# Kernel tuning notes

Measured on AMD Instinct MI355X. Metric: run time of the kernel, lower is better.

The kernel has to match this reference:

```python
import jax, jax.numpy as jnp
import numpy as np
import math

B, H, S, D = 1, 8, 2048, 64
LAMBDA_INIT = 0.8 - 0.6 * math.exp(-0.3)  # depth=1
EPS = 1e-5


def _clin(xr, xi, wr, wi, br, bi):
    # complex linear: (wr + i*wi)(xr + i*xi)
    out_r = xr @ wr.T - xi @ wi.T + br
    out_i = xr @ wi.T + xi @ wr.T + bi
    return out_r, out_i


def setup_inputs() -> dict:
    ks = jax.random.split(jax.random.key(0), 24)
    n = lambda i, shp, s=1.0: jax.random.normal(ks[i], shp, jnp.float32) * s
    inv = 1.0 / math.sqrt(D)
    return {
        'q_r': n(0, (B, H, S, D)), 'q_i': n(1, (B, H, S, D)),
        'k_r': n(2, (B, H, S, D)), 'k_i': n(3, (B, H, S, D)),
        'v_r': n(4, (B, H, S, D)), 'v_i': n(5, (B, H, S, D)),
        'pe_q_r': n(6, (B, H, S, D)), 'pe_q_i': n(7, (B, H, S, D)),
        'pe_k_r': n(8, (B, H, S, D)), 'pe_k_i': n(9, (B, H, S, D)),
        'qwr': n(10, (2 * D, D), inv), 'qwi': n(11, (2 * D, D), inv),
        'qbr': jnp.zeros(2 * D), 'qbi': jnp.zeros(2 * D),
        'kwr': n(12, (D, D), inv), 'kwi': n(13, (D, D), inv),
        'kbr': jnp.zeros(D), 'kbi': jnp.zeros(D),
        'vwr': n(14, (D, D), inv), 'vwi': n(15, (D, D), inv),
        'vbr': jnp.zeros(D), 'vbi': jnp.zeros(D),
        'gwr': n(16, (D, D), inv), 'gwi': n(17, (D, D), inv),
        'gbr': jnp.zeros(D), 'gbi': jnp.zeros(D),
        'owr': n(18, (D, D), inv), 'owi': n(19, (D, D), inv),
        'obr': jnp.zeros(D), 'obi': jnp.zeros(D),
        'lq1': n(20, (H,), 0.1), 'lk1': n(21, (H,), 0.1),
        'lq2': n(22, (H,), 0.1), 'lk2': n(23, (H,), 0.1),
        'subw': jnp.ones(2 * D),
    }


def _forward(q_r, q_i, k_r, k_i, v_r, v_i, pe_q_r, pe_q_i, pe_k_r, pe_k_i,
             qwr, qwi, qbr, qbi, kwr, kwi, kbr, kbi, vwr, vwi, vbr, vbi,
             gwr, gwi, gbr, gbi, owr, owi, obr, obi,
             lq1, lk1, lq2, lk2, subw):
    b, h, s, d = q_r.shape
    scale = d ** (-0.5)
    qpr, qpi = _clin(q_r, q_i, qwr, qwi, qbr, qbi)      # [b,h,s,2d]
    kpr, kpi = _clin(k_r, k_i, kwr, kwi, kbr, kbi)      # [b,h,s,d]
    vpr, vpi = _clin(v_r, v_i, vwr, vwi, vbr, vbi)      # [b,h,s,d]
    qpr = qpr + jnp.concatenate([pe_q_r, pe_q_r], -1)
    qpi = qpi + jnp.concatenate([pe_q_i, pe_q_i], -1)
    kpr = kpr + pe_k_r
    kpi = kpi + pe_k_i
    # split two physical heads: view(..., d, 2) interleaves last dim
    qpr = qpr.reshape(b, h, s, d, 2)
    qpi = qpi.reshape(b, h, s, d, 2)
    q1r, q2r = qpr[..., 0], qpr[..., 1]
    q1i, q2i = qpi[..., 0], qpi[..., 1]

    def attn(qr, qi):
        sr = jnp.einsum('bhqd,bhkd->bhqk', qr, kpr) + jnp.einsum('bhqd,bhkd->bhqk', qi, kpi)
        si = jnp.einsum('bhqd,bhkd->bhqk', qi, kpr) - jnp.einsum('bhqd,bhkd->bhqk', qr, kpi)
        scores = jnp.sqrt(sr * sr + si * si + 1e-8) * scale
        return jax.nn.softmax(scores, axis=-1)

    a1 = attn(q1r, q1i)
    a2 = attn(q2r, q2i)
    o1r = a1 @ vpr; o1i = a1 @ vpi
    o2r = a2 @ vpr; o2i = a2 @ vpi
    # NOTE: torch computes a lambda-weighted difference here but immediately
    # overwrites it with the normed slice below, so it never reaches the output.
    cr = jnp.stack([o1r, o2r], -1).reshape(b, h, s, 2 * d)
    ci = jnp.stack([o1i, o2i], -1).reshape(b, h, s, 2 * d)
    rms = jnp.sqrt(jnp.mean(cr * cr + ci * ci, axis=-1, keepdims=True) + EPS)
    nr = cr / rms * subw
    ni = ci / rms * subw
    ar = nr[..., :d]
    ai = ni[..., :d]
    gr, gi = _clin(q_r, q_i, gwr, gwi, gbr, gbi)
    xr = gr * ar - gi * ai
    xi = gr * ai + gi * ar
    out_r, out_i = _clin(xr, xi, owr, owi, obr, obi)
    return out_r, out_i, gr, gi


def reference(q_r, q_i, k_r, k_i, v_r, v_i, pe_q_r, pe_q_i, pe_k_r, pe_k_i,
              qwr, qwi, qbr, qbi, kwr, kwi, kbr, kbi, vwr, vwi, vbr, vbi,
              gwr, gwi, gbr, gbi, owr, owi, obr, obi,
              lq1, lk1, lq2, lk2, subw):
    return _forward(q_r, q_i, k_r, k_i, v_r, v_i, pe_q_r, pe_q_i, pe_k_r, pe_k_i,
                    qwr, qwi, qbr, qbi, kwr, kwi, kbr, kbi, vwr, vwi, vbr, vbi,
                    gwr, gwi, gbr, gbi, owr, owi, obr, obi,
                    lq1, lk1, lq2, lk2, subw)
```

## Files before the change

### kernel.cpp

```cpp
#include <hip/hip_runtime.h>
#include <hip/hip_bf16.h>

#define NH 8
#define SQ 2048
#define HD 64
#define NTOT (NH * SQ * HD)

typedef unsigned short u16;
typedef unsigned int u32;
typedef __attribute__((ext_vector_type(8))) unsigned short us8;
typedef __attribute__((ext_vector_type(4))) unsigned short us4v;
typedef __attribute__((ext_vector_type(8))) _Float16 h8;
typedef __attribute__((ext_vector_type(4))) float f4;
typedef __attribute__((ext_vector_type(4))) u32 u4;

#define MFMA_F16 __builtin_amdgcn_mfma_f32_16x16x32_f16

__device__ __forceinline__ u16 f2h(float f) {
    union { _Float16 h; u16 u; } c; c.h = (_Float16)f; return c.u;
}
__device__ __forceinline__ float h2f(u16 u) {
    union { _Float16 h; u16 u; } c; c.u = u; return (float)c.h;
}
__device__ __forceinline__ h8 neg_h8(h8 a) {
    union { h8 h; u4 u; } c; c.h = a;
    c.u ^= 0x80008000u;
    return c.h;
}
__device__ __forceinline__ h8 pack8h(const float* p) {
    float4 a = ((const float4*)p)[0];
    float4 b = ((const float4*)p)[1];
    h8 r;
    r[0] = (_Float16)a.x; r[1] = (_Float16)a.y; r[2] = (_Float16)a.z; r[3] = (_Float16)a.w;
    r[4] = (_Float16)b.x; r[5] = (_Float16)b.y; r[6] = (_Float16)b.z; r[7] = (_Float16)b.w;
    return r;
}

__device__ __forceinline__ int swz8(int row, int chunk) {
    return row * 64 + ((chunk ^ (row & 7)) << 3);
}

struct Afrag { h8 r0, r1, i0, i1, ni0, ni1; };

__global__ __launch_bounds__(128) void prep1_kernel(
    const float* __restrict__ qwr, const float* __restrict__ qwi,
    const float* __restrict__ kwr, const float* __restrict__ kwi,
    const float* __restrict__ vwr, const float* __restrict__ vwi,
    const float* __restrict__ gwr, const float* __restrict__ gwi,
    u16* __restrict__ pk)
{
    const int b = blockIdx.x;
    const float* W; int nt;
    if (b < 8)       { W = qwr; nt = b; }
    else if (b < 16) { W = qwi; nt = b - 8; }
    else if (b < 20) { W = kwr; nt = b - 16; }
    else if (b < 24) { W = kwi; nt = b - 20; }
    else if (b < 28) { W = vwr; nt = b - 24; }
    else if (b < 32) { W = vwi; nt = b - 28; }
    else if (b < 36) { W = gwr; nt = b - 32; }
    else             { W = gwi; nt = b - 36; }
    const int t = threadIdx.x, hf = t >> 6, l = t & 63;
    const int quad = l >> 4, m16 = l & 15;
    h8 v = pack8h(W + (nt * 16 + m16) * 64 + hf * 32 + quad * 8);
    *(h8*)(pk + b * 1024 + hf * 512 + l * 8) = v;
}

__global__ __launch_bounds__(128) void prep2_kernel(
    const float* __restrict__ owr, const float* __restrict__ owi,
    u16* __restrict__ pk)
{
    const int b = blockIdx.x;
    const float* W = (b < 4) ? owr : owi;
    const int nt = b & 3;
    const int t = threadIdx.x, hf = t >> 6, l = t & 63;
    const int quad = l >> 4, m16 = l & 15;
    h8 v = pack8h(W + (nt * 16 + m16) * 64 + hf * 32 + quad * 8);
    *(h8*)(pk + b * 1024 + hf * 512 + l * 8) = v;
}

__global__ __launch_bounds__(256) void proj_kernel(
    const float* __restrict__ q_r, const float* __restrict__ q_i,
    const float* __restrict__ k_r, const float* __restrict__ k_i,
    const float* __restrict__ v_r, const float* __restrict__ v_i,
    const float* __restrict__ pe_q_r, const float* __restrict__ pe_q_i,
    const float* __restrict__ pe_k_r, const float* __restrict__ pe_k_i,
    const u16* __restrict__ pk,
    const float* __restrict__ qbr, const float* __restrict__ qbi,
    const float* __restrict__ kbr, const float* __restrict__ kbi,
    const float* __restrict__ vbr, const float* __restrict__ vbi,
    const float* __restrict__ gbr, const float* __restrict__ gbi,
    u16* __restrict__ q1r, u16* __restrict__ q1i,
    u16* __restrict__ q2r, u16* __restrict__ q2i,
    u16* __restrict__ kpr, u16* __restrict__ kpi,
    u16* __restrict__ vtr, u16* __restrict__ vti,
    float* __restrict__ out_gr, float* __restrict__ out_gi)
{
    __shared__ __align__(16) u16 Sqr[16 * 64], Sqi[16 * 64];
    __shared__ __align__(16) u16 Skr[16 * 64], Ski[16 * 64];
    __shared__ __align__(16) u16 Svr[16 * 64], Svi[16 * 64];

    const int t = threadIdx.x;
    const int wv = t >> 6, l = t & 63;
    const int quad = l >> 4, m16 = l & 15;
    const int rowbase = blockIdx.x * 16;
    const int h = rowbase >> 11;
    const int l8 = l * 8;

    {
        const int r = t >> 4, c4 = (t & 15) * 4;
        const int off = swz8(r, c4 >> 3) + (c4 & 7);
        const size_t gi = (size_t)(rowbase + r) * 64 + c4;
        auto stage = [&](const float* src, u16* dst) {
            float4 v = *(const float4*)(src + gi);
            us4v p;
            p[0] = f2h(v.x); p[1] = f2h(v.y); p[2] = f2h(v.z); p[3] = f2h(v.w);
            *(us4v*)&dst[off] = p;
        };
        stage(q_r, Sqr); stage(q_i, Sqi);
        stage(k_r, Skr); stage(k_i, Ski);
        stage(v_r, Svr); stage(v_i, Svi);
    }
    __syncthreads();

    auto loadA = [&](const u16* Sr, const u16* Si) {
        Afrag a;
        a.r0 = *(const h8*)&Sr[swz8(m16, quad)];
        a.r1 = *(const h8*)&Sr[swz8(m16, quad + 4)];
        a.i0 = *(const h8*)&Si[swz8(m16, quad)];
        a.i1 = *(const h8*)&Si[swz8(m16, quad + 4)];
        a.ni0 = neg_h8(a.i0);
        a.ni1 = neg_h8(a.i1);
        return a;
    };

    auto ctile = [&](const Afrag& A, int planeR, int planeI, f4& Cr, f4& Ci) {
        const u16* pR = pk + planeR * 1024;
        const u16* pI = pk + planeI * 1024;
        h8 Br0 = *(const h8*)(pR + l8);
        h8 Br1 = *(const h8*)(pR + 512 + l8);
        h8 Bi0 = *(const h8*)(pI + l8);
        h8 Bi1 = *(const h8*)(pI + 512 + l8);
        Cr = (f4)0.f; Ci = (f4)0.f;
        Cr = MFMA_F16(A.r0,  Br0, Cr, 0, 0, 0);
        Cr = MFMA_F16(A.r1,  Br1, Cr, 0, 0, 0);
        Cr = MFMA_F16(A.ni0, Bi0, Cr, 0, 0, 0);
        Cr = MFMA_F16(A.ni1, Bi1, Cr, 0, 0, 0);
        Ci = MFMA_F16(A.r0,  Bi0, Ci, 0, 0, 0);
        Ci = MFMA_F16(A.r1,  Bi1, Ci, 0, 0, 0);
        Ci = MFMA_F16(A.i0,  Br0, Ci, 0, 0, 0);
        Ci = MFMA_F16(A.i1,  Br1, Ci, 0, 0, 0);
    };

    auto qtile = [&](const Afrag& A, int nt) {
        f4 Cr, Ci;
        ctile(A, nt, 8 + nt, Cr, Ci);
        int c = nt * 16 + m16;
        float br = qbr[c], bi = qbi[c];
        int dd = c >> 1, pc = c & 63;
        u16* dR = (c & 1) ? q2r : q1r;
        u16* dI = (c & 1) ? q2i : q1i;
        #pragma unroll
        for (int r = 0; r < 4; ++r) {
            int g = rowbase + quad * 4 + r;
            dR[g * 64 + dd] = f2h(Cr[r] + br + pe_q_r[g * 64 + pc]);
            dI[g * 64 + dd] = f2h(Ci[r] + bi + pe_q_i[g * 64 + pc]);
        }
    };
    auto ktile = [&](const Afrag& A, int nt) {
        f4 Cr, Ci;
        ctile(A, 16 + nt, 20 + nt, Cr, Ci);
        int c = nt * 16 + m16;
        float br = kbr[c], bi = kbi[c];
        #pragma unroll
        for (int r = 0; r < 4; ++r) {
            int g = rowbase + quad * 4 + r;
            kpr[g * 64 + c] = f2h(Cr[r] + br + pe_k_r[g * 64 + c]);
            kpi[g * 64 + c] = f2h(Ci[r] + bi + pe_k_i[g * 64 + c]);
        }
    };
    auto vtile = [&](const Afrag& A, int nt) {
        f4 Cr, Ci;
        ctile(A, 24 + nt, 28 + nt, Cr, Ci);
        int c = nt * 16 + m16;
        float br = vbr[c], bi = vbi[c];
        int s0 = (rowbase & 2047) + quad * 4;
        size_t tix = (size_t)(h * 64 + c) * 2048 + s0;
        us4v pr, pi;
        #pragma unroll
        for (int r = 0; r < 4; ++r) {
            pr[r] = f2h(Cr[r] + br);
            pi[r] = f2h(Ci[r] + bi);
        }
        *(us4v*)&vtr[tix] = pr;
        *(us4v*)&vti[tix] = pi;
    };
    auto gtile = [&](const Afrag& A, int nt) {
        f4 Cr, Ci;
        ctile(A, 32 + nt, 36 + nt, Cr, Ci);
        int c = nt * 16 + m16;
        float br = gbr[c], bi = gbi[c];
        #pragma unroll
        for (int r = 0; r < 4; ++r) {
            int g = rowbase + quad * 4 + r;
            out_gr[g * 64 + c] = Cr[r] + br;
            out_gi[g * 64 + c] = Ci[r] + bi;
        }
    };

    if (wv == 0) {
        Afrag Aq = loadA(Sqr, Sqi);
        qtile(Aq, 0); qtile(Aq, 1); qtile(Aq, 2); qtile(Aq, 3); qtile(Aq, 4);
    } else if (wv == 1) {
        Afrag Aq = loadA(Sqr, Sqi);
        qtile(Aq, 5); qtile(Aq, 6); qtile(Aq, 7);
        gtile(Aq, 0); gtile(Aq, 1);
    } else if (wv == 2) {
        Afrag Ak = loadA(Skr, Ski);
        ktile(Ak, 0); ktile(Ak, 1); ktile(Ak, 2); ktile(Ak, 3);
        Afrag Aq = loadA(Sqr, Sqi);
        gtile(Aq, 2);
    } else {
        Afrag Av = loadA(Svr, Svi);
        vtile(Av, 0); vtile(Av, 1); vtile(Av, 2); vtile(Av, 3);
        Afrag Aq = loadA(Sqr, Sqi);
        gtile(Aq, 3);
    }
}

__global__ __launch_bounds__(512, 2) void attn_kernel(
    const u16* __restrict__ q1r, const u16* __restrict__ q1i,
    const u16* __restrict__ q2r, const u16* __restrict__ q2i,
    const u16* __restrict__ kpr, const u16* __restrict__ kpi,
    const u16* __restrict__ vtr, const u16* __restrict__ vti,
    u16* __restrict__ o1r, u16* __restrict__ o1i,
    u16* __restrict__ o2r, u16* __restrict__ o2i)
{
    __shared__ __align__(16) u16 Kr[2][64 * 64], Ki[2][64 * 64];
    __shared__ __align__(16) u16 Vr[2][64 * 64], Vi[2][64 * 64];
    __shared__ __align__(16) u16 Pb[128 * 64];

    const int t  = threadIdx.x;
    const int qt = blockIdx.x;
    const int h  = blockIdx.z;

    const int wq   = t >> 6;
    const int br   = wq >> 2;
    const int wr   = wq & 3;
    const int l    = t & 63;
    const int quad = l >> 4;
    const int m    = l & 15;

    const u16* Qsr = br ? q2r : q1r;
    const u16* Qsi = br ? q2i : q1i;
    const int hbase = h * SQ * 64;
    const int qbase = hbase + qt * 64 * 64;
    const int vbase = h * 64 * SQ;

    const u16* qrr = Qsr + qbase + (wr * 16 + m) * 64;
    const u16* qri = Qsi + qbase + (wr * 16 + m) * 64;
    h8 Qr0 = *(const h8*)(qrr + quad * 8);
    h8 Qr1 = *(const h8*)(qrr + 32 + quad * 8);
    h8 Qi0 = *(const h8*)(qri + quad * 8);
    h8 Qi1 = *(const h8*)(qri + 32 + quad * 8);
    h8 nQr0 = neg_h8(Qr0);
    h8 nQr1 = neg_h8(Qr1);

    const int sr0 = t >> 3;
    const int sc  = t & 7;
    us8 rK, rC, rV, rW;

    auto issue = [&](int kt) {
        const int kb = hbase + kt * 4096;
        const int vb = vbase + kt * 64;
        const int sc8 = sc * 8;
        rK = *(const us8*)(kpr + kb + sr0 * 64 + sc8);
        rC = *(const us8*)(kpi + kb + sr0 * 64 + sc8);
        rV = *(const us8*)(vtr + vb + sr0 * SQ + sc8);
        rW = *(const us8*)(vti + vb + sr0 * SQ + sc8);
    };
    auto commit = [&](int b) {
        const int o = swz8(sr0, sc);
        *(us8*)&Kr[b][o] = rK;
        *(us8*)&Ki[b][o] = rC;
        *(us8*)&Vr[b][o] = rV;
        *(us8*)&Vi[b][o] = rW;
    };

    float mreg[4], Lp[4];
    #pragma unroll
    for (int r = 0; r < 4; ++r) { mreg[r] = -1e30f; Lp[r] = 0.f; }
    f4 Ovr[4], Ovi[4];
    #pragma unroll
    for (int d = 0; d < 4; ++d) { Ovr[d] = (f4)0.f; Ovi[d] = (f4)0.f; }

    issue(0);
    commit(0);
    issue(1);
    __syncthreads();

    for (int kt = 0; kt < 32; ++kt) {
        const int cur = kt & 1;
        if (kt < 31) commit(cur ^ 1);
        if (kt < 30) issue(kt + 2);

        float sv[4][4];
        #pragma unroll
        for (int nt = 0; nt < 4; ++nt) {
            const int kr = nt * 16 + m;
            h8 k0 = *(const h8*)&Kr[cur][swz8(kr, quad)];
            h8 k1 = *(const h8*)&Kr[cur][swz8(kr, quad + 4)];
            h8 c0 = *(const h8*)&Ki[cur][swz8(kr, quad)];
            h8 c1 = *(const h8*)&Ki[cur][swz8(kr, quad + 4)];
            f4 ar = (f4)0.f, ai = (f4)0.f;
            __builtin_amdgcn_s_setprio(1);
            ar = MFMA_F16(Qr0, k0, ar, 0, 0, 0);
            ar = MFMA_F16(Qr1, k1, ar, 0, 0, 0);
            ar = MFMA_F16(Qi0, c0, ar, 0, 0, 0);
            ar = MFMA_F16(Qi1, c1, ar, 0, 0, 0);
            ai = MFMA_F16(Qi0, k0, ai, 0, 0, 0);
            ai = MFMA_F16(Qi1, k1, ai, 0, 0, 0);
            ai = MFMA_F16(nQr0, c0, ai, 0, 0, 0);
            ai = MFMA_F16(nQr1, c1, ai, 0, 0, 0);
            __builtin_amdgcn_s_setprio(0);
            #pragma unroll
            for (int r = 0; r < 4; ++r)
                sv[nt][r] = __builtin_amdgcn_sqrtf(ar[r] * ar[r] + ai[r] * ai[r] + 1e-8f) * 0.125f;
        }

        float rv[4];
        #pragma unroll
        for (int r = 0; r < 4; ++r) {
            float x = fmaxf(fmaxf(sv[0][r], sv[1][r]), fmaxf(sv[2][r], sv[3][r]));
            x = fmaxf(x, __shfl_xor(x, 1));
            x = fmaxf(x, __shfl_xor(x, 2));
            x = fmaxf(x, __shfl_xor(x, 4));
            x = fmaxf(x, __shfl_xor(x, 8));
            rv[r] = x;
        }

        bool need = (rv[0] > mreg[0] + 8.f) | (rv[1] > mreg[1] + 8.f) |
                    (rv[2] > mreg[2] + 8.f) | (rv[3] > mreg[3] + 8.f);
        if (__any(need)) {
            #pragma unroll
            for (int r = 0; r < 4; ++r) {
                float mn = fmaxf(mreg[r], rv[r]);
                float al = __expf(mreg[r] - mn);
                mreg[r] = mn;
                Lp[r] *= al;
                #pragma unroll
                for (int dtr = 0; dtr < 4; ++dtr) { Ovr[dtr][r] *= al; Ovi[dtr][r] *= al; }
            }
        }

        #pragma unroll
        for (int r = 0; r < 4; ++r) {
            const int prow = wq * 16 + quad * 4 + r;
            #pragma unroll
            for (int nt = 0; nt < 4; ++nt) {
                float p = __expf(sv[nt][r] - mreg[r]);
                Lp[r] += p;
                const int col = nt * 16 + m;
                Pb[swz8(prow, col >> 3) + (col & 7)] = f2h(p);
            }
        }

        const int qrow = wq * 16 + m;
        h8 pa0 = *(const h8*)&Pb[swz8(qrow, quad)];
        h8 pa1 = *(const h8*)&Pb[swz8(qrow, quad + 4)];

        #pragma unroll
        for (int dt = 0; dt < 4; ++dt) {
            const int vr_ = dt * 16 + m;
            h8 b0 = *(const h8*)&Vr[cur][swz8(vr_, quad)];
            h8 b1 = *(const h8*)&Vr[cur][swz8(vr_, quad + 4)];
            h8 d0 = *(const h8*)&Vi[cur][swz8(vr_, quad)];
            h8 d1 = *(const h8*)&Vi[cur][swz8(vr_, quad + 4)];
            __builtin_amdgcn_s_setprio(1);
            Ovr[dt] = MFMA_F16(pa0, b0, Ovr[dt], 0, 0, 0);
            Ovr[dt] = MFMA_F16(pa1, b1, Ovr[dt], 0, 0, 0);
            Ovi[dt] = MFMA_F16(pa0, d0, Ovi[dt], 0, 0, 0);
            Ovi[dt] = MFMA_F16(pa1, d1, Ovi[dt], 0, 0, 0);
            __builtin_amdgcn_s_setprio(0);
        }

        __syncthreads();
    }

    {
        #pragma unroll
        for (int r = 0; r < 4; ++r) {
            float x = Lp[r];
            x += __shfl_xor(x, 1);
            x += __shfl_xor(x, 2);
            x += __shfl_xor(x, 4);
            x += __shfl_xor(x, 8);
            Lp[r] = x;
        }
        u16* Dr = br ? o2r : o1r;
        u16* Di = br ? o2i : o1i;
        float inv[4];
        #pragma unroll
        for (int r = 0; r < 4; ++r) inv[r] = 1.f / Lp[r];
        #pragma unroll
        for (int dt = 0; dt < 4; ++dt) {
            #pragma unroll
            for (int r = 0; r < 4; ++r) {
                int q = wr * 16 + quad * 4 + r;
                Dr[qbase + q * 64 + dt * 16 + m] = f2h(Ovr[dt][r] * inv[r]);
                Di[qbase + q * 64 + dt * 16 + m] = f2h(Ovi[dt][r] * inv[r]);
            }
        }
    }
}

__global__ __launch_bounds__(256) void epi_kernel(
    const u16* __restrict__ o1r, const u16* __restrict__ o1i,
    const u16* __restrict__ o2r, const u16* __restrict__ o2i,
    const float* __restrict__ out_gr, const float* __restrict__ out_gi,
    const float* __restrict__ subw,
    const u16* __restrict__ pko,
    const float* __restrict__ obr, const float* __restrict__ obi,
    float* __restrict__ out_r, float* __restrict__ out_i)
{
    __shared__ __align__(16) u16 L1r[16][64], L1i[16][64];
    __shared__ __align__(16) u16 L2r[16][64], L2i[16][64];
    __shared__ __align__(16) u16 Xr[16 * 64], Xi[16 * 64];

    const int t = threadIdx.x;
    const int rowbase = blockIdx.x * 16;

    {
        int r = t >> 4, c4 = (t & 15) * 4;
        size_t gi = (size_t)(rowbase + r) * 64 + c4;
        *(us4v*)&L1r[r][c4] = *(const us4v*)(o1r + gi);
        *(us4v*)&L1i[r][c4] = *(const us4v*)(o1i + gi);
        *(us4v*)&L2r[r][c4] = *(const us4v*)(o2r + gi);
        *(us4v*)&L2i[r][c4] = *(const us4v*)(o2i + gi);
    }
    __syncthreads();

    {
        int r = t >> 4, c4 = (t & 15) * 4;
        float ss = 0.f;
        #pragma unroll
        for (int j = 0; j < 4; ++j) {
            float a = h2f(L1r[r][c4 + j]), b = h2f(L1i[r][c4 + j]);
            float c = h2f(L2r[r][c4 + j]), d = h2f(L2i[r][c4 + j]);
            ss += a * a + b * b + c * c + d * d;
        }
        ss += __shfl_xor(ss, 1);
        ss += __shfl_xor(ss, 2);
        ss += __shfl_xor(ss, 4);
        ss += __shfl_xor(ss, 8);
        float inv = 1.f / sqrtf(ss * (1.f / 128.f) + 1e-5f);

        float4 g_r = *(const float4*)(out_gr + (size_t)(rowbase + r) * 64 + c4);
        float4 g_i = *(const float4*)(out_gi + (size_t)(rowbase + r) * 64 + c4);
        const float* grv = (const float*)&g_r;
        const float* giv = (const float*)&g_i;

        us4v xrp, xip;
        #pragma unroll
        for (int j = 0; j < 4; ++j) {
            int c = c4 + j;
            int s = c >> 1;
            float cr_ = (c & 1) ? h2f(L2r[r][s]) : h2f(L1r[r][s]);
            float ci_ = (c & 1) ? h2f(L2i[r][s]) : h2f(L1i[r][s]);
            float sw = subw[c];
            float ar_ = cr_ * inv * sw;
            float ai_ = ci_ * inv * sw;
            xrp[j] = f2h(grv[j] * ar_ - giv[j] * ai_);
            xip[j] = f2h(grv[j] * ai_ + giv[j] * ar_);
        }
        const int off = swz8(r, c4 >> 3) + (c4 & 7);
        *(us4v*)&Xr[off] = xrp;
        *(us4v*)&Xi[off] = xip;
    }
    __syncthreads();

    const int wv = t >> 6, l = t & 63;
    const int quad = l >> 4, m16 = l & 15;
    const int l8 = l * 8;

    h8 Ar0 = *(const h8*)&Xr[swz8(m16, quad)];
    h8 Ar1 = *(const h8*)&Xr[swz8(m16, quad + 4)];
    h8 Ai0 = *(const h8*)&Xi[swz8(m16, quad)];
    h8 Ai1 = *(const h8*)&Xi[swz8(m16, quad + 4)];
    h8 nAi0 = neg_h8(Ai0), nAi1 = neg_h8(Ai1);

    const int c = wv * 16 + m16;
    h8 Br0 = *(const h8*)(pko + wv * 1024 + l8);
    h8 Br1 = *(const h8*)(pko + wv * 1024 + 512 + l8);
    h8 Bi0 = *(const h8*)(pko + 4096 + wv * 1024 + l8);
    h8 Bi1 = *(const h8*)(pko + 4096 + wv * 1024 + 512 + l8);

    f4 Cr = (f4)0.f, Ci = (f4)0.f;
    Cr = MFMA_F16(Ar0,  Br0, Cr, 0, 0, 0);
    Cr = MFMA_F16(Ar1,  Br1, Cr, 0, 0, 0);
    Cr = MFMA_F16(nAi0, Bi0, Cr, 0, 0, 0);
    Cr = MFMA_F16(nAi1, Bi1, Cr, 0, 0, 0);
    Ci = MFMA_F16(Ar0,  Bi0, Ci, 0, 0, 0);
    Ci = MFMA_F16(Ar1,  Bi1, Ci, 0, 0, 0);
    Ci = MFMA_F16(Ai0,  Br0, Ci, 0, 0, 0);
    Ci = MFMA_F16(Ai1,  Br1, Ci, 0, 0, 0);

    float br_ = obr[c], bi_ = obi[c];
    #pragma unroll
    for (int r = 0; r < 4; ++r) {
        size_t g = (size_t)(rowbase + quad * 4 + r) * 64 + c;
        out_r[g] = Cr[r] + br_;
        out_i[g] = Ci[r] + bi_;
    }
}

extern "C" void kernel_launch(void* const* d_in, const int* in_sizes, int n_in,
                              void* d_out, int out_size, void* d_ws, size_t ws_size,
                              hipStream_t stream)
{
    (void)in_sizes; (void)n_in; (void)out_size; (void)ws_size;

    float* out    = (float*)d_out;
    float* out_r  = out;
    float* out_i  = out + (size_t)NTOT;
    float* out_gr = out + 2 * (size_t)NTOT;
    float* out_gi = out + 3 * (size_t)NTOT;

    char* w = (char*)d_ws;
    const size_t N = (size_t)NTOT;
    u16* q1r = (u16*)w; w += N * 2;
    u16* q1i = (u16*)w; w += N * 2;
    u16* q2r = (u16*)w; w += N * 2;
    u16* q2i = (u16*)w; w += N * 2;
    u16* kpr = (u16*)w; w += N * 2;
    u16* kpi = (u16*)w; w += N * 2;
    u16* vtr = (u16*)w; w += N * 2;
    u16* vti = (u16*)w; w += N * 2;
    u16* o1r = (u16*)w; w += N * 2;
    u16* o1i = (u16*)w; w += N * 2;
    u16* o2r = (u16*)w; w += N * 2;
    u16* o2i = (u16*)w; w += N * 2;

    u16* pk1 = o1r;
    u16* pk2 = q1r;

    prep1_kernel<<<dim3(40), dim3(128), 0, stream>>>(
        (const float*)d_in[10], (const float*)d_in[11],
        (const float*)d_in[14], (const float*)d_in[15],
        (const float*)d_in[18], (const float*)d_in[19],
        (const float*)d_in[22], (const float*)d_in[23],
        pk1);

    proj_kernel<<<dim3(1024), dim3(256), 0, stream>>>(
        (const float*)d_in[0], (const float*)d_in[1],
        (const float*)d_in[2], (const float*)d_in[3],
        (const float*)d_in[4], (const float*)d_in[5],
        (const float*)d_in[6], (const float*)d_in[7],
        (const float*)d_in[8], (const float*)d_in[9],
        pk1,
        (const float*)d_in[12], (const float*)d_in[13],
        (const float*)d_in[16], (const float*)d_in[17],
        (const float*)d_in[20], (const float*)d_in[21],
        (const float*)d_in[24], (const float*)d_in[25],
        q1r, q1i, q2r, q2i, kpr, kpi, vtr, vti, out_gr, out_gi);

    attn_kernel<<<dim3(SQ / 64, 1, NH), dim3(512), 0, stream>>>(
        q1r, q1i, q2r, q2i, kpr, kpi, vtr, vti, o1r, o1i, o2r, o2i);

    prep2_kernel<<<dim3(8), dim3(128), 0, stream>>>(
        (const float*)d_in[26], (const float*)d_in[27], pk2);

    epi_kernel<<<dim3(1024), dim3(256), 0, stream>>>(
        o1r, o1i, o2r, o2i, out_gr, out_gi,
        (const float*)d_in[34], pk2,
        (const float*)d_in[28], (const float*)d_in[29],
        out_r, out_i);
}
```

Measured before the change: 236.1 us.

## Split KV tiles across two wave groups with 32-row waves and merged softmax

Each wave now handles 32 query rows instead of 16, so every K/V fragment read from LDS feeds twice as many MFMAs. The two halves of the block process alternating KV tiles from a triple-buffered LDS ring and merge their partial max, sum and output through LDS scratch at the end. This aims to cut LDS read traffic per MFMA and expose more independent work. In exchange, LDS use grows to about 128KB, which likely allows only one block per CU despite the launch bound of 2, and each iteration now has an extra barrier.

```diff
diff --git a/kernel.cpp b/kernel.cpp
--- a/kernel.cpp
+++ b/kernel.cpp
@@ -235,17 +235,17 @@
     u16* __restrict__ o1r, u16* __restrict__ o1i,
     u16* __restrict__ o2r, u16* __restrict__ o2i)
 {
-    __shared__ __align__(16) u16 Kr[2][64 * 64], Ki[2][64 * 64];
-    __shared__ __align__(16) u16 Vr[2][64 * 64], Vi[2][64 * 64];
-    __shared__ __align__(16) u16 Pb[128 * 64];
+    __shared__ __align__(16) u16 TILE[3][4][4096];
+    __shared__ __align__(16) u16 Pb[256 * 64];
 
     const int t  = threadIdx.x;
     const int qt = blockIdx.x;
     const int h  = blockIdx.z;
 
     const int wq   = t >> 6;
-    const int br   = wq >> 2;
-    const int wr   = wq & 3;
+    const int grp  = wq >> 2;
+    const int br   = (wq >> 1) & 1;
+    const int rh   = wq & 1;
     const int l    = t & 63;
     const int quad = l >> 4;
     const int m    = l & 15;
@@ -256,158 +256,232 @@
     const int qbase = hbase + qt * 64 * 64;
     const int vbase = h * 64 * SQ;
 
-    const u16* qrr = Qsr + qbase + (wr * 16 + m) * 64;
-    const u16* qri = Qsi + qbase + (wr * 16 + m) * 64;
-    h8 Qr0 = *(const h8*)(qrr + quad * 8);
-    h8 Qr1 = *(const h8*)(qrr + 32 + quad * 8);
-    h8 Qi0 = *(const h8*)(qri + quad * 8);
-    h8 Qi1 = *(const h8*)(qri + 32 + quad * 8);
-    h8 nQr0 = neg_h8(Qr0);
-    h8 nQr1 = neg_h8(Qr1);
+    h8 Qr0[2], Qr1[2], Qi0[2], Qi1[2];
+    #pragma unroll
+    for (int rs = 0; rs < 2; ++rs) {
+        const u16* qrr = Qsr + qbase + (rh * 32 + rs * 16 + m) * 64;
+        const u16* qri = Qsi + qbase + (rh * 32 + rs * 16 + m) * 64;
+        Qr0[rs] = *(const h8*)(qrr + quad * 8);
+        Qr1[rs] = *(const h8*)(qrr + 32 + quad * 8);
+        Qi0[rs] = *(const h8*)(qri + quad * 8);
+        Qi1[rs] = *(const h8*)(qri + 32 + quad * 8);
+    }
 
     const int sr0 = t >> 3;
     const int sc  = t & 7;
-    us8 rK, rC, rV, rW;
-
-    auto issue = [&](int kt) {
+    us8 rKa, rCa, rVa, rWa;
+    us8 rKb, rCb, rVb, rWb;
+
+    auto issueT = [&](int kt, us8& K, us8& C, us8& V, us8& W) {
         const int kb = hbase + kt * 4096;
         const int vb = vbase + kt * 64;
         const int sc8 = sc * 8;
-        rK = *(const us8*)(kpr + kb + sr0 * 64 + sc8);
-        rC = *(const us8*)(kpi + kb + sr0 * 64 + sc8);
-        rV = *(const us8*)(vtr + vb + sr0 * SQ + sc8);
-        rW = *(const us8*)(vti + vb + sr0 * SQ + sc8);
-    };
-    auto commit = [&](int b) {
+        K = *(const us8*)(kpr + kb + sr0 * 64 + sc8);
+        C = *(const us8*)(kpi + kb + sr0 * 64 + sc8);
+        V = *(const us8*)(vtr + vb + sr0 * SQ + sc8);
+        W = *(const us8*)(vti + vb + sr0 * SQ + sc8);
+    };
+    auto commitT = [&](int slot, const us8& K, const us8& C, const us8& V, const us8& W) {
         const int o = swz8(sr0, sc);
-        *(us8*)&Kr[b][o] = rK;
-        *(us8*)&Ki[b][o] = rC;
-        *(us8*)&Vr[b][o] = rV;
-        *(us8*)&Vi[b][o] = rW;
-    };
-
-    float mreg[4], Lp[4];
+        *(us8*)&TILE[slot][0][o] = K;
+        *(us8*)&TILE[slot][1][o] = C;
+        *(us8*)&TILE[slot][2][o] = V;
+        *(us8*)&TILE[slot][3][o] = W;
+    };
+
+    float mreg[2][4], Lp[2][4];
     #pragma unroll
-    for (int r = 0; r < 4; ++r) { mreg[r] = -1e30f; Lp[r] = 0.f; }
-    f4 Ovr[4], Ovi[4];
+    for (int rs = 0; rs < 2; ++rs)
+        #pragma unroll
+        for (int r = 0; r < 4; ++r) { mreg[rs][r] = -1e30f; Lp[rs][r] = 0.f; }
+    f4 Ovr[2][4], Ovi[2][4];
     #pragma unroll
-    for (int d = 0; d < 4; ++d) { Ovr[d] = (f4)0.f; Ovi[d] = (f4)0.f; }
-
-    issue(0);
-    commit(0);
-    issue(1);
+    for (int rs = 0; rs < 2; ++rs)
+        #pragma unroll
+        for (int d = 0; d < 4; ++d) { Ovr[rs][d] = (f4)0.f; Ovi[rs][d] = (f4)0.f; }
+
+    issueT(0, rKa, rCa, rVa, rWa);
+    issueT(1, rKb, rCb, rVb, rWb);
+    commitT(0, rKa, rCa, rVa, rWa);
+    issueT(2, rKa, rCa, rVa, rWa);
+    commitT(1, rKb, rCb, rVb, rWb);
+    issueT(3, rKb, rCb, rVb, rWb);
     __syncthreads();
 
-    for (int kt = 0; kt < 32; ++kt) {
-        const int cur = kt & 1;
-        if (kt < 31) commit(cur ^ 1);
-        if (kt < 30) issue(kt + 2);
-
-        float sv[4][4];
+    for (int s = 0; s < 16; ++s) {
+        const int myt  = 2 * s + grp;
+        const int slot = myt % 3;
+        if (s < 15) commitT((2 * s + 2) % 3, rKa, rCa, rVa, rWa);
+        if (s < 14) issueT(2 * s + 4, rKa, rCa, rVa, rWa);
+
+        const u16* Kr_ = TILE[slot][0];
+        const u16* Ki_ = TILE[slot][1];
+        const u16* Vr_ = TILE[slot][2];
+        const u16* Vi_ = TILE[slot][3];
+
+        float sv[2][4][4];
         #pragma unroll
         for (int nt = 0; nt < 4; ++nt) {
             const int kr = nt * 16 + m;
-            h8 k0 = *(const h8*)&Kr[cur][swz8(kr, quad)];
-            h8 k1 = *(const h8*)&Kr[cur][swz8(kr, quad + 4)];
-            h8 c0 = *(const h8*)&Ki[cur][swz8(kr, quad)];
-            h8 c1 = *(const h8*)&Ki[cur][swz8(kr, quad + 4)];
-            f4 ar = (f4)0.f, ai = (f4)0.f;
+            h8 k0 = *(const h8*)&Kr_[swz8(kr, quad)];
+            h8 k1 = *(const h8*)&Kr_[swz8(kr, quad + 4)];
+            h8 c0 = *(const h8*)&Ki_[swz8(kr, quad)];
+            h8 c1 = *(const h8*)&Ki_[swz8(kr, quad + 4)];
+            h8 nc0 = neg_h8(c0);
+            h8 nc1 = neg_h8(c1);
             __builtin_amdgcn_s_setprio(1);
-            ar = MFMA_F16(Qr0, k0, ar, 0, 0, 0);
-            ar = MFMA_F16(Qr1, k1, ar, 0, 0, 0);
-            ar = MFMA_F16(Qi0, c0, ar, 0, 0, 0);
-            ar = MFMA_F16(Qi1, c1, ar, 0, 0, 0);
-            ai = MFMA_F16(Qi0, k0, ai, 0, 0, 0);
-            ai = MFMA_F16(Qi1, k1, ai, 0, 0, 0);
-            ai = MFMA_F16(nQr0, c0, ai, 0, 0, 0);
-            ai = MFMA_F16(nQr1, c1, ai, 0, 0, 0);
+            #pragma unroll
+            for (int rs = 0; rs < 2; ++rs) {
+                f4 ar = (f4)0.f, ai = (f4)0.f;
+                ar = MFMA_F16(Qr0[rs], k0, ar, 0, 0, 0);
+                ar = MFMA_F16(Qr1[rs], k1, ar, 0, 0, 0);
+                ar = MFMA_F16(Qi0[rs], c0, ar, 0, 0, 0);
+                ar = MFMA_F16(Qi1[rs], c1, ar, 0, 0, 0);
+                ai = MFMA_F16(Qi0[rs], k0, ai, 0, 0, 0);
+                ai = MFMA_F16(Qi1[rs], k1, ai, 0, 0, 0);
+                ai = MFMA_F16(Qr0[rs], nc0, ai, 0, 0, 0);
+                ai = MFMA_F16(Qr1[rs], nc1, ai, 0, 0, 0);
+                #pragma unroll
+                for (int r = 0; r < 4; ++r)
+                    sv[rs][nt][r] =
+                        __builtin_amdgcn_sqrtf(ar[r] * ar[r] + ai[r] * ai[r] + 1e-8f) * 0.125f;
+            }
             __builtin_amdgcn_s_setprio(0);
-            #pragma unroll
-            for (int r = 0; r < 4; ++r)
-                sv[nt][r] = __builtin_amdgcn_sqrtf(ar[r] * ar[r] + ai[r] * ai[r] + 1e-8f) * 0.125f;
-        }
-
-        float rv[4];
-        #pragma unroll
-        for (int r = 0; r < 4; ++r) {
-            float x = fmaxf(fmaxf(sv[0][r], sv[1][r]), fmaxf(sv[2][r], sv[3][r]));
-            x = fmaxf(x, __shfl_xor(x, 1));
-            x = fmaxf(x, __shfl_xor(x, 2));
-            x = fmaxf(x, __shfl_xor(x, 4));
-            x = fmaxf(x, __shfl_xor(x, 8));
-            rv[r] = x;
-        }
-
-        bool need = (rv[0] > mreg[0] + 8.f) | (rv[1] > mreg[1] + 8.f) |
-                    (rv[2] > mreg[2] + 8.f) | (rv[3] > mreg[3] + 8.f);
+        }
+
+        float rv[2][4];
+        bool need = false;
+        #pragma unroll
+        for (int rs = 0; rs < 2; ++rs)
+            #pragma unroll
+            for (int r = 0; r < 4; ++r) {
+                float x = fmaxf(fmaxf(sv[rs][0][r], sv[rs][1][r]),
+                                fmaxf(sv[rs][2][r], sv[rs][3][r]));
+                x = fmaxf(x, __shfl_xor(x, 1));
+                x = fmaxf(x, __shfl_xor(x, 2));
+                x = fmaxf(x, __shfl_xor(x, 4));
+                x = fmaxf(x, __shfl_xor(x, 8));
+                rv[rs][r] = x;
+                need |= (x > mreg[rs][r] + 8.f);
+            }
         if (__any(need)) {
             #pragma unroll
+            for (int rs = 0; rs < 2; ++rs)
+                #pragma unroll
+                for (int r = 0; r < 4; ++r) {
+                    float mn = fmaxf(mreg[rs][r], rv[rs][r]);
+                    float al = __expf(mreg[rs][r] - mn);
+                    mreg[rs][r] = mn;
+                    Lp[rs][r] *= al;
+                    #pragma unroll
+                    for (int dt = 0; dt < 4; ++dt) {
+                        Ovr[rs][dt][r] *= al; Ovi[rs][dt][r] *= al;
+                    }
+                }
+        }
+
+        #pragma unroll
+        for (int rs = 0; rs < 2; ++rs)
+            #pragma unroll
             for (int r = 0; r < 4; ++r) {
-                float mn = fmaxf(mreg[r], rv[r]);
-                float al = __expf(mreg[r] - mn);
-                mreg[r] = mn;
-                Lp[r] *= al;
+                const int prow = wq * 32 + rs * 16 + quad * 4 + r;
                 #pragma unroll
-                for (int dtr = 0; dtr < 4; ++dtr) { Ovr[dtr][r] *= al; Ovi[dtr][r] *= al; }
+                for (int nt = 0; nt < 4; ++nt) {
+                    float p = __expf(sv[rs][nt][r] - mreg[rs][r]);
+                    Lp[rs][r] += p;
+                    const int col = nt * 16 + m;
+                    Pb[swz8(prow, col >> 3) + (col & 7)] = f2h(p);
+                }
             }
-        }
-
-        #pragma unroll
-        for (int r = 0; r < 4; ++r) {
-            const int prow = wq * 16 + quad * 4 + r;
-            #pragma unroll
-            for (int nt = 0; nt < 4; ++nt) {
-                float p = __expf(sv[nt][r] - mreg[r]);
-                Lp[r] += p;
-                const int col = nt * 16 + m;
-                Pb[swz8(prow, col >> 3) + (col & 7)] = f2h(p);
+
+        h8 pa0[2], pa1[2];
+        #pragma unroll
+        for (int rs = 0; rs < 2; ++rs) {
+            const int qrow = wq * 32 + rs * 16 + m;
+            pa0[rs] = *(const h8*)&Pb[swz8(qrow, quad)];
+            pa1[rs] = *(const h8*)&Pb[swz8(qrow, quad + 4)];
+        }
+
+        #pragma unroll
+        for (int dt = 0; dt < 4; ++dt) {
+            const int vrr = dt * 16 + m;
+            h8 b0 = *(const h8*)&Vr_[swz8(vrr, quad)];
+            h8 b1 = *(const h8*)&Vr_[swz8(vrr, quad + 4)];
+            h8 d0 = *(const h8*)&Vi_[swz8(vrr, quad)];
+            h8 d1 = *(const h8*)&Vi_[swz8(vrr, quad + 4)];
+            __builtin_amdgcn_s_setprio(1);
+            #pragma unroll
+            for (int rs = 0; rs < 2; ++rs) {
+                Ovr[rs][dt] = MFMA_F16(pa0[rs], b0, Ovr[rs][dt], 0, 0, 0);
+                Ovr[rs][dt] = MFMA_F16(pa1[rs], b1, Ovr[rs][dt], 0, 0, 0);
+                Ovi[rs][dt] = MFMA_F16(pa0[rs], d0, Ovi[rs][dt], 0, 0, 0);
+                Ovi[rs][dt] = MFMA_F16(pa1[rs], d1, Ovi[rs][dt], 0, 0, 0);
             }
-        }
-
-        const int qrow = wq * 16 + m;
-        h8 pa0 = *(const h8*)&Pb[swz8(qrow, quad)];
-        h8 pa1 = *(const h8*)&Pb[swz8(qrow, quad + 4)];
-
-        #pragma unroll
-        for (int dt = 0; dt < 4; ++dt) {
-            const int vr_ = dt * 16 + m;
-            h8 b0 = *(const h8*)&Vr[cur][swz8(vr_, quad)];
-            h8 b1 = *(const h8*)&Vr[cur][swz8(vr_, quad + 4)];
-            h8 d0 = *(const h8*)&Vi[cur][swz8(vr_, quad)];
-            h8 d1 = *(const h8*)&Vi[cur][swz8(vr_, quad + 4)];
-            __builtin_amdgcn_s_setprio(1);
-            Ovr[dt] = MFMA_F16(pa0, b0, Ovr[dt], 0, 0, 0);
-            Ovr[dt] = MFMA_F16(pa1, b1, Ovr[dt], 0, 0, 0);
-            Ovi[dt] = MFMA_F16(pa0, d0, Ovi[dt], 0, 0, 0);
-            Ovi[dt] = MFMA_F16(pa1, d1, Ovi[dt], 0, 0, 0);
             __builtin_amdgcn_s_setprio(0);
         }
 
         __syncthreads();
-    }
-
-    {
-        #pragma unroll
-        for (int r = 0; r < 4; ++r) {
-            float x = Lp[r];
-            x += __shfl_xor(x, 1);
-            x += __shfl_xor(x, 2);
-            x += __shfl_xor(x, 4);
-            x += __shfl_xor(x, 8);
-            Lp[r] = x;
-        }
+        if (s < 15) commitT((2 * s + 3) % 3, rKb, rCb, rVb, rWb);
+        if (s < 14) issueT(2 * s + 5, rKb, rCb, rVb, rWb);
+        __syncthreads();
+    }
+
+    float* scr = (float*)&TILE[0][0][0];
+    const int sbase = ((wq & 3) * 64 + l) * 80;
+    if (grp == 1) {
+        #pragma unroll
+        for (int rs = 0; rs < 2; ++rs) {
+            #pragma unroll
+            for (int dt = 0; dt < 4; ++dt)
+                #pragma unroll
+                for (int r = 0; r < 4; ++r) {
+                    scr[sbase + rs * 32 + dt * 8 + r * 2 + 0] = Ovr[rs][dt][r];
+                    scr[sbase + rs * 32 + dt * 8 + r * 2 + 1] = Ovi[rs][dt][r];
+                }
+            #pragma unroll
+            for (int r = 0; r < 4; ++r) {
+                scr[sbase + 64 + rs * 8 + r * 2 + 0] = mreg[rs][r];
+                scr[sbase + 64 + rs * 8 + r * 2 + 1] = Lp[rs][r];
+            }
+        }
+    }
+    __syncthreads();
+    if (grp == 0) {
         u16* Dr = br ? o2r : o1r;
         u16* Di = br ? o2i : o1i;
-        float inv[4];
-        #pragma unroll
-        for (int r = 0; r < 4; ++r) inv[r] = 1.f / Lp[r];
-        #pragma unroll
-        for (int dt = 0; dt < 4; ++dt) {
+        #pragma unroll
+        for (int rs = 0; rs < 2; ++rs) {
+            float inv[4];
             #pragma unroll
             for (int r = 0; r < 4; ++r) {
-                int q = wr * 16 + quad * 4 + r;
-                Dr[qbase + q * 64 + dt * 16 + m] = f2h(Ovr[dt][r] * inv[r]);
-                Di[qbase + q * 64 + dt * 16 + m] = f2h(Ovi[dt][r] * inv[r]);
+                float mB = scr[sbase + 64 + rs * 8 + r * 2 + 0];
+                float LB = scr[sbase + 64 + rs * 8 + r * 2 + 1];
+                float mn = fmaxf(mreg[rs][r], mB);
+                float aA = __expf(mreg[rs][r] - mn);
+                float aB = __expf(mB - mn);
+                float Lm = Lp[rs][r] * aA + LB * aB;
+                #pragma unroll
+                for (int dt = 0; dt < 4; ++dt) {
+                    float obr_ = scr[sbase + rs * 32 + dt * 8 + r * 2 + 0];
+                    float obi_ = scr[sbase + rs * 32 + dt * 8 + r * 2 + 1];
+                    Ovr[rs][dt][r] = Ovr[rs][dt][r] * aA + obr_ * aB;
+                    Ovi[rs][dt][r] = Ovi[rs][dt][r] * aA + obi_ * aB;
+                }
+                float x = Lm;
+                x += __shfl_xor(x, 1);
+                x += __shfl_xor(x, 2);
+                x += __shfl_xor(x, 4);
+                x += __shfl_xor(x, 8);
+                inv[r] = 1.f / x;
+            }
+            #pragma unroll
+            for (int dt = 0; dt < 4; ++dt) {
+                #pragma unroll
+                for (int r = 0; r < 4; ++r) {
+                    int q = rh * 32 + rs * 16 + quad * 4 + r;
+                    Dr[qbase + q * 64 + dt * 16 + m] = f2h(Ovr[rs][dt][r] * inv[r]);
+                    Di[qbase + q * 64 + dt * 16 + m] = f2h(Ovi[rs][dt][r] * inv[r]);
+                }
             }
         }
     }
```

Measured after the change: 283.8 us. 1.2x slower.

## Fuse RMS-norm, gating and output projection epilogue into attention kernel

Applied to the files above, without the earlier changes.

Moves the sub-layer RMS normalization, complex gating and output complex linear into the tail of the attention kernel. The two branch outputs are combined through a shared-memory sum-of-squares, and the gated result is staged in the P buffer for MFMA. This removes the fp16 o1/o2 intermediate round trip through global memory, the separate epilogue launch and the second weight-prep launch, since all weights are now packed in one prep kernel. It also changes attention launch bounds from 2 to 1 waves-per-EU minimum, which may allow more registers but can reduce occupancy.

```diff
diff --git a/kernel.cpp b/kernel.cpp
--- a/kernel.cpp
+++ b/kernel.cpp
@@ -42,11 +42,12 @@
 
 struct Afrag { h8 r0, r1, i0, i1, ni0, ni1; };
 
-__global__ __launch_bounds__(128) void prep1_kernel(
+__global__ __launch_bounds__(128) void prep_kernel(
     const float* __restrict__ qwr, const float* __restrict__ qwi,
     const float* __restrict__ kwr, const float* __restrict__ kwi,
     const float* __restrict__ vwr, const float* __restrict__ vwi,
     const float* __restrict__ gwr, const float* __restrict__ gwi,
+    const float* __restrict__ owr, const float* __restrict__ owi,
     u16* __restrict__ pk)
 {
     const int b = blockIdx.x;
@@ -58,20 +59,9 @@
     else if (b < 28) { W = vwr; nt = b - 24; }
     else if (b < 32) { W = vwi; nt = b - 28; }
     else if (b < 36) { W = gwr; nt = b - 32; }
-    else             { W = gwi; nt = b - 36; }
-    const int t = threadIdx.x, hf = t >> 6, l = t & 63;
-    const int quad = l >> 4, m16 = l & 15;
-    h8 v = pack8h(W + (nt * 16 + m16) * 64 + hf * 32 + quad * 8);
-    *(h8*)(pk + b * 1024 + hf * 512 + l * 8) = v;
-}
-
-__global__ __launch_bounds__(128) void prep2_kernel(
-    const float* __restrict__ owr, const float* __restrict__ owi,
-    u16* __restrict__ pk)
-{
-    const int b = blockIdx.x;
-    const float* W = (b < 4) ? owr : owi;
-    const int nt = b & 3;
+    else if (b < 40) { W = gwi; nt = b - 36; }
+    else if (b < 44) { W = owr; nt = b - 40; }
+    else             { W = owi; nt = b - 44; }
     const int t = threadIdx.x, hf = t >> 6, l = t & 63;
     const int quad = l >> 4, m16 = l & 15;
     h8 v = pack8h(W + (nt * 16 + m16) * 64 + hf * 32 + quad * 8);
@@ -227,17 +217,21 @@
     }
 }
 
-__global__ __launch_bounds__(512, 2) void attn_kernel(
+__global__ __launch_bounds__(512, 1) void attn_kernel(
     const u16* __restrict__ q1r, const u16* __restrict__ q1i,
     const u16* __restrict__ q2r, const u16* __restrict__ q2i,
     const u16* __restrict__ kpr, const u16* __restrict__ kpi,
     const u16* __restrict__ vtr, const u16* __restrict__ vti,
-    u16* __restrict__ o1r, u16* __restrict__ o1i,
-    u16* __restrict__ o2r, u16* __restrict__ o2i)
+    const u16* __restrict__ pk,
+    const float* __restrict__ subw,
+    const float* __restrict__ obr, const float* __restrict__ obi,
+    const float* __restrict__ out_gr, const float* __restrict__ out_gi,
+    float* __restrict__ out_r, float* __restrict__ out_i)
 {
     __shared__ __align__(16) u16 Kr[2][64 * 64], Ki[2][64 * 64];
     __shared__ __align__(16) u16 Vr[2][64 * 64], Vi[2][64 * 64];
     __shared__ __align__(16) u16 Pb[128 * 64];
+    __shared__ float ssL[2][64];
 
     const int t  = threadIdx.x;
     const int qt = blockIdx.x;
@@ -394,122 +388,100 @@
             x += __shfl_xor(x, 2);
             x += __shfl_xor(x, 4);
             x += __shfl_xor(x, 8);
-            Lp[r] = x;
-        }
-        u16* Dr = br ? o2r : o1r;
-        u16* Di = br ? o2i : o1i;
-        float inv[4];
-        #pragma unroll
-        for (int r = 0; r < 4; ++r) inv[r] = 1.f / Lp[r];
-        #pragma unroll
-        for (int dt = 0; dt < 4; ++dt) {
+            float inv = 1.f / x;
+            #pragma unroll
+            for (int dt = 0; dt < 4; ++dt) { Ovr[dt][r] *= inv; Ovi[dt][r] *= inv; }
+        }
+
+        float ssp[4];
+        #pragma unroll
+        for (int r = 0; r < 4; ++r) {
+            float s = 0.f;
+            #pragma unroll
+            for (int dt = 0; dt < 4; ++dt)
+                s += Ovr[dt][r] * Ovr[dt][r] + Ovi[dt][r] * Ovi[dt][r];
+            s += __shfl_xor(s, 1);
+            s += __shfl_xor(s, 2);
+            s += __shfl_xor(s, 4);
+            s += __shfl_xor(s, 8);
+            ssp[r] = s;
+        }
+        if (m == 0) {
+            #pragma unroll
+            for (int r = 0; r < 4; ++r)
+                ssL[br][wr * 16 + quad * 4 + r] = ssp[r];
+        }
+        __syncthreads();
+
+        float rmi[4];
+        #pragma unroll
+        for (int r = 0; r < 4; ++r) {
+            const int row = wr * 16 + quad * 4 + r;
+            float ss = ssL[0][row] + ssL[1][row];
+            rmi[r] = 1.f / sqrtf(ss * (1.f / 128.f) + 1e-5f);
+        }
+
+        u16* Xr = Pb;
+        u16* Xi = Pb + 4096;
+        const int growb = h * 2048 + qt * 64;
+        #pragma unroll
+        for (int dt = 0; dt < 2; ++dt) {
+            const int k = dt * 16 + m;
+            const int c = 2 * k + br;
+            const float sw = subw[c];
             #pragma unroll
             for (int r = 0; r < 4; ++r) {
-                int q = wr * 16 + quad * 4 + r;
-                Dr[qbase + q * 64 + dt * 16 + m] = f2h(Ovr[dt][r] * inv[r]);
-                Di[qbase + q * 64 + dt * 16 + m] = f2h(Ovi[dt][r] * inv[r]);
+                const int row = wr * 16 + quad * 4 + r;
+                const size_t gidx = (size_t)(growb + row) * 64 + c;
+                float g_r = out_gr[gidx];
+                float g_i = out_gi[gidx];
+                float a_r = Ovr[dt][r] * rmi[r] * sw;
+                float a_i = Ovi[dt][r] * rmi[r] * sw;
+                const int off = swz8(row, c >> 3) + (c & 7);
+                Xr[off] = f2h(g_r * a_r - g_i * a_i);
+                Xi[off] = f2h(g_r * a_i + g_i * a_r);
             }
         }
-    }
-}
-
-__global__ __launch_bounds__(256) void epi_kernel(
-    const u16* __restrict__ o1r, const u16* __restrict__ o1i,
-    const u16* __restrict__ o2r, const u16* __restrict__ o2i,
-    const float* __restrict__ out_gr, const float* __restrict__ out_gi,
-    const float* __restrict__ subw,
-    const u16* __restrict__ pko,
-    const float* __restrict__ obr, const float* __restrict__ obi,
-    float* __restrict__ out_r, float* __restrict__ out_i)
-{
-    __shared__ __align__(16) u16 L1r[16][64], L1i[16][64];
-    __shared__ __align__(16) u16 L2r[16][64], L2i[16][64];
-    __shared__ __align__(16) u16 Xr[16 * 64], Xi[16 * 64];
-
-    const int t = threadIdx.x;
-    const int rowbase = blockIdx.x * 16;
-
-    {
-        int r = t >> 4, c4 = (t & 15) * 4;
-        size_t gi = (size_t)(rowbase + r) * 64 + c4;
-        *(us4v*)&L1r[r][c4] = *(const us4v*)(o1r + gi);
-        *(us4v*)&L1i[r][c4] = *(const us4v*)(o1i + gi);
-        *(us4v*)&L2r[r][c4] = *(const us4v*)(o2r + gi);
-        *(us4v*)&L2i[r][c4] = *(const us4v*)(o2i + gi);
-    }
-    __syncthreads();
-
-    {
-        int r = t >> 4, c4 = (t & 15) * 4;
-        float ss = 0.f;
-        #pragma unroll
-        for (int j = 0; j < 4; ++j) {
-            float a = h2f(L1r[r][c4 + j]), b = h2f(L1i[r][c4 + j]);
-            float c = h2f(L2r[r][c4 + j]), d = h2f(L2i[r][c4 + j]);
-            ss += a * a + b * b + c * c + d * d;
-        }
-        ss += __shfl_xor(ss, 1);
-        ss += __shfl_xor(ss, 2);
-        ss += __shfl_xor(ss, 4);
-        ss += __shfl_xor(ss, 8);
-        float inv = 1.f / sqrtf(ss * (1.f / 128.f) + 1e-5f);
-
-        float4 g_r = *(const float4*)(out_gr + (size_t)(rowbase + r) * 64 + c4);
-        float4 g_i = *(const float4*)(out_gi + (size_t)(rowbase + r) * 64 + c4);
-        const float* grv = (const float*)&g_r;
-        const float* giv = (const float*)&g_i;
-
-        us4v xrp, xip;
-        #pragma unroll
-        for (int j = 0; j < 4; ++j) {
-            int c = c4 + j;
-            int s = c >> 1;
-            float cr_ = (c & 1) ? h2f(L2r[r][s]) : h2f(L1r[r][s]);
-            float ci_ = (c & 1) ? h2f(L2i[r][s]) : h2f(L1i[r][s]);
-            float sw = subw[c];
-            float ar_ = cr_ * inv * sw;
-            float ai_ = ci_ * inv * sw;
-            xrp[j] = f2h(grv[j] * ar_ - giv[j] * ai_);
-            xip[j] = f2h(grv[j] * ai_ + giv[j] * ar_);
-        }
-        const int off = swz8(r, c4 >> 3) + (c4 & 7);
-        *(us4v*)&Xr[off] = xrp;
-        *(us4v*)&Xi[off] = xip;
-    }
-    __syncthreads();
-
-    const int wv = t >> 6, l = t & 63;
-    const int quad = l >> 4, m16 = l & 15;
-    const int l8 = l * 8;
-
-    h8 Ar0 = *(const h8*)&Xr[swz8(m16, quad)];
-    h8 Ar1 = *(const h8*)&Xr[swz8(m16, quad + 4)];
-    h8 Ai0 = *(const h8*)&Xi[swz8(m16, quad)];
-    h8 Ai1 = *(const h8*)&Xi[swz8(m16, quad + 4)];
-    h8 nAi0 = neg_h8(Ai0), nAi1 = neg_h8(Ai1);
-
-    const int c = wv * 16 + m16;
-    h8 Br0 = *(const h8*)(pko + wv * 1024 + l8);
-    h8 Br1 = *(const h8*)(pko + wv * 1024 + 512 + l8);
-    h8 Bi0 = *(const h8*)(pko + 4096 + wv * 1024 + l8);
-    h8 Bi1 = *(const h8*)(pko + 4096 + wv * 1024 + 512 + l8);
-
-    f4 Cr = (f4)0.f, Ci = (f4)0.f;
-    Cr = MFMA_F16(Ar0,  Br0, Cr, 0, 0, 0);
-    Cr = MFMA_F16(Ar1,  Br1, Cr, 0, 0, 0);
-    Cr = MFMA_F16(nAi0, Bi0, Cr, 0, 0, 0);
-    Cr = MFMA_F16(nAi1, Bi1, Cr, 0, 0, 0);
-    Ci = MFMA_F16(Ar0,  Bi0, Ci, 0, 0, 0);
-    Ci = MFMA_F16(Ar1,  Bi1, Ci, 0, 0, 0);
-    Ci = MFMA_F16(Ai0,  Br0, Ci, 0, 0, 0);
-    Ci = MFMA_F16(Ai1,  Br1, Ci, 0, 0, 0);
-
-    float br_ = obr[c], bi_ = obi[c];
-    #pragma unroll
-    for (int r = 0; r < 4; ++r) {
-        size_t g = (size_t)(rowbase + quad * 4 + r) * 64 + c;
-        out_r[g] = Cr[r] + br_;
-        out_i[g] = Ci[r] + bi_;
+        __syncthreads();
+
+        const int ct  = wq & 3;
+        const int rh2 = wq >> 2;
+        const int c   = ct * 16 + m;
+        const float br_ = obr[c], bi_ = obi[c];
+        const u16* pR = pk + (40 + ct) * 1024;
+        const u16* pI = pk + (44 + ct) * 1024;
+        h8 Br0 = *(const h8*)(pR + l * 8);
+        h8 Br1 = *(const h8*)(pR + 512 + l * 8);
+        h8 Bi0 = *(const h8*)(pI + l * 8);
+        h8 Bi1 = *(const h8*)(pI + 512 + l * 8);
+
+        #pragma unroll
+        for (int rt = 0; rt < 2; ++rt) {
+            const int arow = rh2 * 32 + rt * 16 + m;
+            h8 Ar0 = *(const h8*)&Xr[swz8(arow, quad)];
+            h8 Ar1 = *(const h8*)&Xr[swz8(arow, quad + 4)];
+            h8 Ai0 = *(const h8*)&Xi[swz8(arow, quad)];
+            h8 Ai1 = *(const h8*)&Xi[swz8(arow, quad + 4)];
+            h8 nAi0 = neg_h8(Ai0), nAi1 = neg_h8(Ai1);
+
+            f4 Cr = (f4)0.f, Ci = (f4)0.f;
+            Cr = MFMA_F16(Ar0,  Br0, Cr, 0, 0, 0);
+            Cr = MFMA_F16(Ar1,  Br1, Cr, 0, 0, 0);
+            Cr = MFMA_F16(nAi0, Bi0, Cr, 0, 0, 0);
+            Cr = MFMA_F16(nAi1, Bi1, Cr, 0, 0, 0);
+            Ci = MFMA_F16(Ar0,  Bi0, Ci, 0, 0, 0);
+            Ci = MFMA_F16(Ar1,  Bi1, Ci, 0, 0, 0);
+            Ci = MFMA_F16(Ai0,  Br0, Ci, 0, 0, 0);
+            Ci = MFMA_F16(Ai1,  Br1, Ci, 0, 0, 0);
+
+            #pragma unroll
+            for (int r = 0; r < 4; ++r) {
+                const int row = rh2 * 32 + rt * 16 + quad * 4 + r;
+                const size_t g = (size_t)(growb + row) * 64 + c;
+                out_r[g] = Cr[r] + br_;
+                out_i[g] = Ci[r] + bi_;
+            }
+        }
     }
 }
 
@@ -535,20 +507,15 @@
     u16* kpi = (u16*)w; w += N * 2;
     u16* vtr = (u16*)w; w += N * 2;
     u16* vti = (u16*)w; w += N * 2;
-    u16* o1r = (u16*)w; w += N * 2;
-    u16* o1i = (u16*)w; w += N * 2;
-    u16* o2r = (u16*)w; w += N * 2;
-    u16* o2i = (u16*)w; w += N * 2;
-
-    u16* pk1 = o1r;
-    u16* pk2 = q1r;
-
-    prep1_kernel<<<dim3(40), dim3(128), 0, stream>>>(
+    u16* pk  = (u16*)w;
+
+    prep_kernel<<<dim3(48), dim3(128), 0, stream>>>(
         (const float*)d_in[10], (const float*)d_in[11],
         (const float*)d_in[14], (const float*)d_in[15],
         (const float*)d_in[18], (const float*)d_in[19],
         (const float*)d_in[22], (const float*)d_in[23],
-        pk1);
+        (const float*)d_in[26], (const float*)d_in[27],
+        pk);
 
     proj_kernel<<<dim3(1024), dim3(256), 0, stream>>>(
         (const float*)d_in[0], (const float*)d_in[1],
@@ -556,7 +523,7 @@
         (const float*)d_in[4], (const float*)d_in[5],
         (const float*)d_in[6], (const float*)d_in[7],
         (const float*)d_in[8], (const float*)d_in[9],
-        pk1,
+        pk,
         (const float*)d_in[12], (const float*)d_in[13],
         (const float*)d_in[16], (const float*)d_in[17],
         (const float*)d_in[20], (const float*)d_in[21],
@@ -564,14 +531,8 @@
         q1r, q1i, q2r, q2i, kpr, kpi, vtr, vti, out_gr, out_gi);
 
     attn_kernel<<<dim3(SQ / 64, 1, NH), dim3(512), 0, stream>>>(
-        q1r, q1i, q2r, q2i, kpr, kpi, vtr, vti, o1r, o1i, o2r, o2i);
-
-    prep2_kernel<<<dim3(8), dim3(128), 0, stream>>>(
-        (const float*)d_in[26], (const float*)d_in[27], pk2);
-
-    epi_kernel<<<dim3(1024), dim3(256), 0, stream>>>(
-        o1r, o1i, o2r, o2i, out_gr, out_gi,
-        (const float*)d_in[34], pk2,
+        q1r, q1i, q2r, q2i, kpr, kpi, vtr, vti,
+        pk, (const float*)d_in[34],
         (const float*)d_in[28], (const float*)d_in[29],
-        out_r, out_i);
-}
+        out_gr, out_gi, out_r, out_i);
+}
```

New measurement: 234.6 us. About the same (-0.6%).
